# Optimization experiments

Hardware: AMD Instinct MI355X
Metric: run time of the kernel (lower is better)

Reference implementation:

```python
import jax, jax.numpy as jnp
import numpy as np

B, L, D, H, F = 4, 2048, 768, 12, 3072
ROUTE_FRAC = 0.15
LN_EPS = 1e-5


def _ln(x, g, b):
    m = jnp.mean(x, axis=-1, keepdims=True)
    v = jnp.mean((x - m) ** 2, axis=-1, keepdims=True)
    return (x - m) * jax.lax.rsqrt(v + LN_EPS) * g + b


def setup_inputs() -> dict:
    key = jax.random.key(0)
    ks = jax.random.split(key, 20)
    s = 0.02
    return {
        "hidden_states": jax.random.normal(ks[0], (B, L, D), dtype=jnp.float32),
        "g1": jnp.ones((D,), jnp.float32), "b1": jnp.zeros((D,), jnp.float32),
        "g2": jnp.ones((D,), jnp.float32), "b2": jnp.zeros((D,), jnp.float32),
        "Wr": jax.random.normal(ks[1], (D,), jnp.float32) * s, "br": jnp.zeros((), jnp.float32),
        "Wq": jax.random.normal(ks[2], (D, D), jnp.float32) * s, "bq": jnp.zeros((D,), jnp.float32),
        "Wk": jax.random.normal(ks[3], (D, D), jnp.float32) * s, "bk": jnp.zeros((D,), jnp.float32),
        "Wv": jax.random.normal(ks[4], (D, D), jnp.float32) * s, "bv": jnp.zeros((D,), jnp.float32),
        "Wo": jax.random.normal(ks[5], (D, D), jnp.float32) * s, "bo": jnp.zeros((D,), jnp.float32),
        "Wm": jax.random.normal(ks[6], (D, D), jnp.float32) * s, "bm": jnp.zeros((D,), jnp.float32),
        "W1": jax.random.normal(ks[7], (D, F), jnp.float32) * s, "bf1": jnp.zeros((F,), jnp.float32),
        "W2": jax.random.normal(ks[8], (F, D), jnp.float32) * s, "bf2": jnp.zeros((D,), jnp.float32),
    }


def reference(hidden_states, g1, b1, g2, b2, Wr, br, Wq, bq, Wk, bk, Wv, bv, Wo, bo, Wm, bm, W1, bf1, W2, bf2):
    b, l, d = hidden_states.shape
    dh = d // H
    normed = _ln(hidden_states, g1, b1)  # [B,L,D]

    # Router: per-token coherence score; lowest-coherence route_frac tokens get attention.
    scores = jax.nn.sigmoid(jnp.einsum('bld,d->bl', normed, Wr) + br)  # [B,L]
    k = max(1, int(round(ROUTE_FRAC * l)))
    _, idx = jax.lax.top_k(-scores, k)  # lowest-coherence token indices
    attn_mask = jnp.zeros((b, l), bool).at[jnp.arange(b)[:, None], idx].set(True)

    # Attention path (computed densely over all tokens, as the torch module does).
    q = (normed @ Wq + bq).reshape(b, l, H, dh)
    kk = (normed @ Wk + bk).reshape(b, l, H, dh)
    v = (normed @ Wv + bv).reshape(b, l, H, dh)
    logits = jnp.einsum('blhd,bmhd->bhlm', q, kk) / jnp.sqrt(jnp.float32(dh))
    probs = jax.nn.softmax(logits, axis=-1)
    ctx = jnp.einsum('bhlm,bmhd->blhd', probs, v).reshape(b, l, d)
    attn_out = ctx @ Wo + bo

    # Lightweight coherence-mixing path: coherence-weighted global pooling + linear.
    w = scores / (jnp.sum(scores, axis=1, keepdims=True) + 1e-6)
    pooled = jnp.einsum('bl,bld->bd', w, normed)  # [B,D]
    mix_out = (normed + scores[..., None] * pooled[:, None, :]) @ Wm + bm

    merged = jnp.where(attn_mask[..., None], attn_out, mix_out)
    h = hidden_states + merged  # dropout is identity at eval

    n2 = _ln(h, g2, b2)
    ffn = jax.nn.gelu(n2 @ W1 + bf1, approximate=False) @ W2 + bf2
    return h + ffn
```

## Files before the change

### kernel.cpp

```cpp
#include <hip/hip_runtime.h>
#include <math.h>

#define B_ 4
#define L_ 2048
#define D_ 768
#define H_ 12
#define F_ 3072
#define KTOP 307
#define KPAD 320
#define LN_EPS 1e-5f

typedef unsigned int u32;
typedef unsigned short u16;
using bf16x8 = __attribute__((ext_vector_type(8))) short;
using f32x4  = __attribute__((ext_vector_type(4))) float;

#define AS1 __attribute__((address_space(1)))
#define AS3 __attribute__((address_space(3)))

__device__ __forceinline__ void gl16(const void* g, void* l) {
    __builtin_amdgcn_global_load_lds((const AS1 u32*)g, (AS3 u32*)l, 16, 0, 0);
}
__device__ __forceinline__ void wait_vm0() {
    asm volatile("s_waitcnt vmcnt(0)" ::: "memory");
}
__device__ __forceinline__ u16 f2bf(float f) {
    u32 u = __float_as_uint(f);
    return (u16)((u + 0x7fff + ((u >> 16) & 1)) >> 16);
}
__device__ __forceinline__ float bf2f(u16 s) {
    return __uint_as_float(((u32)s) << 16);
}
__device__ __forceinline__ float gelu_tanh(float v) {
    float u = v * v * v;
    float z = fmaf(u, 0.0713548163f, 1.59576912f * v);
    float s = __builtin_amdgcn_rcpf(1.0f + __expf(-z));
    return v * s;
}

__device__ __forceinline__ float blk_reduce_sum(float v, float* red) {
    #pragma unroll
    for (int off = 32; off; off >>= 1) v += __shfl_xor(v, off, 64);
    __syncthreads();
    if ((threadIdx.x & 63) == 0) red[threadIdx.x >> 6] = v;
    __syncthreads();
    return red[0] + red[1] + red[2] + red[3];
}

template <bool SCORE>
__global__ __launch_bounds__(256) void ln_kernel(
    const float* __restrict__ x, const float* __restrict__ g,
    const float* __restrict__ be, const float* __restrict__ Wr,
    const float* __restrict__ brp, u16* __restrict__ outn,
    float* __restrict__ scores)
{
    __shared__ float red[4];
    const int t = blockIdx.x;
    const int tid = threadIdx.x;
    const float* xr = x + (size_t)t * D_;
    float v0 = xr[tid], v1 = xr[tid + 256], v2 = xr[tid + 512];
    float mean = blk_reduce_sum(v0 + v1 + v2, red) * (1.0f / 768.0f);
    float d0 = v0 - mean, d1 = v1 - mean, d2 = v2 - mean;
    __syncthreads();
    float var = blk_reduce_sum(d0 * d0 + d1 * d1 + d2 * d2, red) * (1.0f / 768.0f);
    float inv = 1.0f / sqrtf(var + LN_EPS);
    float n0 = d0 * inv * g[tid] + be[tid];
    float n1 = d1 * inv * g[tid + 256] + be[tid + 256];
    float n2 = d2 * inv * g[tid + 512] + be[tid + 512];
    u16* orow = outn + (size_t)t * D_;
    orow[tid] = f2bf(n0); orow[tid + 256] = f2bf(n1); orow[tid + 512] = f2bf(n2);
    if (SCORE) {
        __syncthreads();
        float dot = blk_reduce_sum(n0 * Wr[tid] + n1 * Wr[tid + 256] + n2 * Wr[tid + 512], red);
        if (tid == 0) scores[t] = 1.0f / (1.0f + expf(-(dot + brp[0])));
    }
}

__global__ __launch_bounds__(1024) void topk_kernel(
    const float* __restrict__ scores, unsigned* __restrict__ mask,
    float* __restrict__ ssum, int* __restrict__ rowmap, int* __restrict__ inv)
{
    __shared__ u32 sb[L_];
    __shared__ u32 hist[256];
    __shared__ u32 wsum[16];
    __shared__ float redf[16];
    __shared__ u32 bcast[2];
    __shared__ u32 cnt_sel;
    const int b = blockIdx.x, tid = threadIdx.x;
    const int lane = tid & 63, wv = tid >> 6;

    if (tid == 0) cnt_sel = 0;
    float s0 = scores[b * L_ + tid];
    float s1 = scores[b * L_ + tid + 1024];
    sb[tid] = __float_as_uint(s0);
    sb[tid + 1024] = __float_as_uint(s1);
    float v = s0 + s1;
    #pragma unroll
    for (int o = 32; o; o >>= 1) v += __shfl_xor(v, o, 64);
    if (lane == 0) redf[wv] = v;
    __syncthreads();
    if (tid == 0) {
        float t = 0.f;
        #pragma unroll
        for (int w = 0; w < 16; w++) t += redf[w];
        ssum[b] = t;
    }

    u32 want = KTOP, prefix = 0;
    #pragma unroll
    for (int pass = 0; pass < 4; pass++) {
        const int shift = 24 - pass * 8;
        if (tid < 256) hist[tid] = 0;
        __syncthreads();
        u32 x0 = sb[tid], x1 = sb[tid + 1024];
        if (pass == 0 || (x0 >> (shift + 8)) == prefix) atomicAdd(&hist[(x0 >> shift) & 255], 1u);
        if (pass == 0 || (x1 >> (shift + 8)) == prefix) atomicAdd(&hist[(x1 >> shift) & 255], 1u);
        __syncthreads();
        u32 c = 0, inc = 0;
        if (tid < 256) {
            c = hist[tid];
            inc = c;
            #pragma unroll
            for (int o = 1; o < 64; o <<= 1) {
                u32 t = __shfl_up(inc, o, 64);
                if (lane >= o) inc += t;
            }
            if (lane == 63) wsum[wv] = inc;
        }
        __syncthreads();
        if (tid < 256) {
            u32 base = 0;
            #pragma unroll
            for (int w = 0; w < 4; w++) if (w < wv) base += wsum[w];
            u32 incl = base + inc;
            u32 excl = incl - c;
            if (excl < want && want <= incl) {
                bcast[0] = (u32)tid;
                bcast[1] = want - excl;
            }
        }
        __syncthreads();
        prefix = (prefix << 8) | bcast[0];
        want = bcast[1];
    }

    const u32 sstar = prefix;
    u32 a0 = sb[2 * tid], a1 = sb[2 * tid + 1];
    u32 e0 = (a0 == sstar) ? 1u : 0u, e1 = (a1 == sstar) ? 1u : 0u;
    u32 ps = e0 + e1, inc2 = ps;
    #pragma unroll
    for (int o = 1; o < 64; o <<= 1) {
        u32 t = __shfl_up(inc2, o, 64);
        if (lane >= o) inc2 += t;
    }
    __syncthreads();
    if (lane == 63) wsum[wv] = inc2;
    __syncthreads();
    u32 base = 0;
    #pragma unroll
    for (int w = 0; w < 16; w++) if (w < wv) base += wsum[w];
    u32 excl0 = base + inc2 - ps;
    {
        int i = 2 * tid;
        bool sel = (a0 < sstar) || (e0 && (excl0 < want));
        mask[b * L_ + i] = sel ? 1u : 0u;
        int invv = 0;
        if (sel) {
            u32 slot = atomicAdd(&cnt_sel, 1u);
            rowmap[b * KPAD + slot] = b * L_ + i;
            invv = b * KPAD + (int)slot;
        }
        inv[b * L_ + i] = invv;
    }
    {
        int i = 2 * tid + 1;
        u32 r1 = excl0 + e0;
        bool sel = (a1 < sstar) || (e1 && (r1 < want));
        mask[b * L_ + i] = sel ? 1u : 0u;
        int invv = 0;
        if (sel) {
            u32 slot = atomicAdd(&cnt_sel, 1u);
            rowmap[b * KPAD + slot] = b * L_ + i;
            invv = b * KPAD + (int)slot;
        }
        inv[b * L_ + i] = invv;
    }
    if (tid < KPAD - KTOP)
        rowmap[b * KPAD + KTOP + tid] = b * L_;
}

__global__ __launch_bounds__(256) void pooled_part(
    const float* __restrict__ scores, const u16* __restrict__ nb,
    float* __restrict__ parts)
{
    const int lc = blockIdx.x, b = blockIdx.y, tid = threadIdx.x;
    float a0 = 0.f, a1 = 0.f, a2 = 0.f;
    for (int l = lc * 256; l < lc * 256 + 256; l++) {
        float s = scores[b * L_ + l];
        const u16* row = nb + (size_t)(b * L_ + l) * D_;
        a0 += s * bf2f(row[tid]);
        a1 += s * bf2f(row[tid + 256]);
        a2 += s * bf2f(row[tid + 512]);
    }
    float* p = parts + (size_t)(lc * B_ + b) * D_;
    p[tid] = a0; p[tid + 256] = a1; p[tid + 512] = a2;
}

__global__ __launch_bounds__(256) void pooled_wm(
    const float* __restrict__ parts, const float* __restrict__ ssum,
    const float* __restrict__ Wm, float* __restrict__ pWm)
{
    __shared__ float pl[768];
    const int b = blockIdx.y, n0 = blockIdx.x * 256, tid = threadIdx.x;
    float inv = 1.0f / (ssum[b] + 1e-6f);
    for (int d = tid; d < 768; d += 256) {
        float s = 0.f;
        #pragma unroll
        for (int lc = 0; lc < 8; lc++) s += parts[(size_t)(lc * B_ + b) * D_ + d];
        pl[d] = s * inv;
    }
    __syncthreads();
    const int n = n0 + tid;
    float acc = 0.f;
    for (int k = 0; k < 768; k++) acc += pl[k] * Wm[(size_t)k * D_ + n];
    pWm[b * D_ + n] = acc;
}

__global__ __launch_bounds__(256) void wconv_all(
    const float* __restrict__ Wq, const float* __restrict__ Wk,
    const float* __restrict__ Wv, const float* __restrict__ Wo,
    const float* __restrict__ Wm, const float* __restrict__ W1,
    const float* __restrict__ W2,
    u16* __restrict__ WqT, u16* __restrict__ WkvT, u16* __restrict__ WoT,
    u16* __restrict__ WmT, u16* __restrict__ W1T, u16* __restrict__ W2T,
    const float* __restrict__ bq, const float* __restrict__ bk,
    const float* __restrict__ bv, float* __restrict__ bqs,
    float* __restrict__ bkv)
{
    __shared__ float t[32][33];
    int id = blockIdx.x;
    const int tid = threadIdx.x;
    if (id >= 7488) {
        for (int i = tid; i < 768; i += 256) {
            bqs[i] = bq[i] * 0.125f;
            bkv[i] = bk[i];
            bkv[768 + i] = bv[i];
        }
        return;
    }
    const float* src; u16* dst; int K, N, local; float sc = 1.f;
    if (id < 576)       { src = Wq; dst = WqT; K = 768; N = 768; local = id; sc = 0.125f; }
    else if (id < 1152) { src = Wk; dst = WkvT;            K = 768; N = 768; local = id - 576; }
    else if (id < 1728) { src = Wv; dst = WkvT + 768 * 768; K = 768; N = 768; local = id - 1152; }
    else if (id < 2304) { src = Wo; dst = WoT; K = 768; N = 768; local = id - 1728; }
    else if (id < 2880) { src = Wm; dst = WmT; K = 768; N = 768; local = id - 2304; }
    else if (id < 5184) { src = W1; dst = W1T; K = 768; N = 3072; local = id - 2880; }
    else                { src = W2; dst = W2T; K = 3072; N = 768; local = id - 5184; }
    const int ntiles = N >> 5;
    const int n0 = (local % ntiles) * 32, k0 = (local / ntiles) * 32;
    const int tx = tid & 31, ty = tid >> 5;
    #pragma unroll
    for (int i = 0; i < 4; i++)
        t[ty + i * 8][tx] = src[(size_t)(k0 + ty + i * 8) * N + n0 + tx];
    __syncthreads();
    #pragma unroll
    for (int i = 0; i < 4; i++)
        dst[(size_t)(n0 + ty + i * 8) * K + k0 + tx] = f2bf(t[tx][ty + i * 8] * sc);
}

template <int EPI, bool RMAP, int TM>
__global__ __launch_bounds__(256) void mfma_gemm(
    const u16* __restrict__ A, const u16* __restrict__ Bt,
    const float* __restrict__ bias, void* __restrict__ Cout,
    int N, int K, int nbn,
    const float* __restrict__ x, const unsigned* __restrict__ msk,
    const float* __restrict__ attn, const float* __restrict__ scores,
    const float* __restrict__ pWm, const float* __restrict__ hres,
    const int* __restrict__ rowmap, const int* __restrict__ invmap)
{
    constexpr int NI = (TM == 128) ? 4 : 2;
    constexpr int ASLOTS = TM * 8 / 256;
    __shared__ u16 Asm[TM * 64];
    __shared__ u16 Bsm[128 * 64];
    const int tid = threadIdx.x;
    const int wave = tid >> 6, lane = tid & 63;
    const int quad = lane >> 4, l15 = lane & 15;

    const int wid = blockIdx.x;
    const int m0 = (wid / nbn) * TM, n0 = (wid % nbn) * 128;
    const int wm = (TM == 128) ? (wave >> 1) * 64 : 0;
    const int wn = (TM == 128) ? (wave & 1) * 64 : wave * 32;

    f32x4 acc[4][NI];
    #pragma unroll
    for (int i = 0; i < 4; i++)
        #pragma unroll
        for (int j = 0; j < NI; j++) acc[i][j] = 0.f;

    const u16* ap[ASLOTS]; const u16* bp[4];
    #pragma unroll
    for (int i = 0; i < ASLOTS; i++) {
        int s = i * 256 + tid;
        int row = s >> 3;
        int kq = (s & 7) ^ (row & 7);
        int arow = RMAP ? rowmap[m0 + row] : (m0 + row);
        ap[i] = A + (size_t)arow * K + kq * 8;
    }
    #pragma unroll
    for (int i = 0; i < 4; i++) {
        int s = i * 256 + tid;
        int row = s >> 3;
        int kq = (s & 7) ^ (row & 7);
        bp[i] = Bt + (size_t)(n0 + row) * K + kq * 8;
    }

    for (int k0 = 0; k0 < K; k0 += 64) {
        #pragma unroll
        for (int i = 0; i < ASLOTS; i++) {
            gl16(ap[i], &Asm[(i * 256 + wave * 64) * 8]);
            ap[i] += 64;
        }
        #pragma unroll
        for (int i = 0; i < 4; i++) {
            gl16(bp[i], &Bsm[(i * 256 + wave * 64) * 8]);
            bp[i] += 64;
        }
        wait_vm0();
        __syncthreads();
        #pragma unroll
        for (int kk = 0; kk < 2; kk++) {
            bf16x8 af[4], bf[NI];
            const int kq = kk * 4 + quad;
            #pragma unroll
            for (int mi = 0; mi < 4; mi++) {
                int row = wm + mi * 16 + l15;
                af[mi] = *(const bf16x8*)&Asm[(row * 8 + (kq ^ (row & 7))) * 8];
            }
            #pragma unroll
            for (int ni = 0; ni < NI; ni++) {
                int row = wn + ni * 16 + l15;
                bf[ni] = *(const bf16x8*)&Bsm[(row * 8 + (kq ^ (row & 7))) * 8];
            }
            #pragma unroll
            for (int mi = 0; mi < 4; mi++)
                #pragma unroll
                for (int ni = 0; ni < NI; ni++)
                    acc[mi][ni] = __builtin_amdgcn_mfma_f32_16x16x32_bf16(
                        af[mi], bf[ni], acc[mi][ni], 0, 0, 0);
        }
        __syncthreads();
    }

    #pragma unroll
    for (int mi = 0; mi < 4; mi++) {
        #pragma unroll
        for (int ni = 0; ni < NI; ni++) {
            #pragma unroll
            for (int r = 0; r < 4; r++) {
                int row = m0 + wm + mi * 16 + quad * 4 + r;
                int col = n0 + wn + ni * 16 + l15;
                float v = acc[mi][ni][r] + bias[col];
                size_t off = (size_t)row * N + col;
                if (EPI == 0) ((float*)Cout)[off] = v;
                else if (EPI == 1) ((u16*)Cout)[off] = f2bf(v);
                else if (EPI == 2) ((u16*)Cout)[off] = f2bf(gelu_tanh(v));
                else if (EPI == 3) {
                    float mix = v + scores[row] * pWm[(row >> 11) * D_ + col];
                    float sel = msk[row] ? attn[(size_t)invmap[row] * D_ + col] : mix;
                    ((float*)Cout)[off] = x[off] + sel;
                } else {
                    ((float*)Cout)[off] = v + hres[off];
                }
            }
        }
    }
}

__global__ __launch_bounds__(256) void vtrans(
    const u16* __restrict__ V, u16* __restrict__ VT, int ld)
{
    __shared__ u16 tl[64 * 72];
    const int tid = threadIdx.x;
    const int l0 = blockIdx.x * 64, h = blockIdx.y, b = blockIdx.z;
    const u16* src = V + h * 64;
    {
        int r = tid >> 3, ch = tid & 7;
        *(uint4*)&tl[r * 72 + ch * 8] =
            *(const uint4*)&src[(size_t)(b * L_ + l0 + r) * ld + ch * 8];
        int t2 = tid + 256; r = t2 >> 3; ch = t2 & 7;
        *(uint4*)&tl[r * 72 + ch * 8] =
            *(const uint4*)&src[(size_t)(b * L_ + l0 + r) * ld + ch * 8];
    }
    __syncthreads();
    int d = tid >> 2, lg = (tid & 3) * 16;
    u16* dst = VT + (size_t)((b * H_ + h) * 64 + d) * L_ + l0 + lg;
    union { u16 s[8]; uint4 v; } pk;
    #pragma unroll
    for (int j = 0; j < 8; j++) pk.s[j] = tl[(lg + j) * 72 + d];
    *(uint4*)dst = pk.v;
    #pragma unroll
    for (int j = 0; j < 8; j++) pk.s[j] = tl[(lg + 8 + j) * 72 + d];
    *(uint4*)(dst + 8) = pk.v;
}

__global__ __launch_bounds__(256) void attn2(
    const u16* __restrict__ qcomp, const u16* __restrict__ Kg,
    const u16* __restrict__ VTg, u16* __restrict__ ctxc)
{
    __shared__ u16 Qs[64 * 64];
    __shared__ u16 Ks[64 * 64];
    __shared__ u16 Vs[64 * 64];
    __shared__ u16 Ps[4 * 16 * 72];
    const int tid = threadIdx.x, wave = tid >> 6, lane = tid & 63;
    const int quad = lane >> 4, l15 = lane & 15;
    const int qb = blockIdx.x, h = blockIdx.y, b = blockIdx.z;
    const int q0 = qb * 64;

    {
        int s0 = wave * 64 + lane;
        int r = s0 >> 3, c = (s0 & 7) ^ (r & 7);
        gl16(qcomp + (size_t)(b * KPAD + q0 + r) * D_ + h * 64 + c * 8,
             &Qs[(wave * 64) * 8]);
        int s1 = s0 + 256;
        int r1 = s1 >> 3, c1 = (s1 & 7) ^ (r1 & 7);
        gl16(qcomp + (size_t)(b * KPAD + q0 + r1) * D_ + h * 64 + c1 * 8,
             &Qs[(256 + wave * 64) * 8]);
    }
    const u16 *kp0, *kp1, *vp0, *vp1;
    {
        int s0 = wave * 64 + lane;
        int r = s0 >> 3, c = (s0 & 7) ^ (r & 7);
        kp0 = Kg + (size_t)(b * L_ + r) * 1536 + h * 64 + c * 8;
        vp0 = VTg + (size_t)((b * H_ + h) * 64 + r) * L_ + c * 8;
        int s1 = s0 + 256;
        int r1 = s1 >> 3, c1 = (s1 & 7) ^ (r1 & 7);
        kp1 = Kg + (size_t)(b * L_ + r1) * 1536 + h * 64 + c1 * 8;
        vp1 = VTg + (size_t)((b * H_ + h) * 64 + r1) * L_ + c1 * 8;
    }
    wait_vm0();
    __syncthreads();
    bf16x8 qf0, qf1;
    {
        int row = wave * 16 + l15;
        qf0 = *(const bf16x8*)&Qs[(row * 8 + ((quad)     ^ (row & 7))) * 8];
        qf1 = *(const bf16x8*)&Qs[(row * 8 + ((4 + quad) ^ (row & 7))) * 8];
    }
    f32x4 accO[4]; float lp[4];
    #pragma unroll
    for (int i = 0; i < 4; i++) { accO[i] = 0.f; lp[i] = 0.f; }
    u16* Psw = Ps + wave * 16 * 72;

    for (int kt = 0; kt < L_; kt += 64) {
        gl16(kp0, &Ks[(wave * 64) * 8]);        kp0 += (size_t)64 * 1536;
        gl16(kp1, &Ks[(256 + wave * 64) * 8]);  kp1 += (size_t)64 * 1536;
        gl16(vp0, &Vs[(wave * 64) * 8]);        vp0 += 64;
        gl16(vp1, &Vs[(256 + wave * 64) * 8]);  vp1 += 64;
        wait_vm0();
        __syncthreads();

        f32x4 accS[4];
        #pragma unroll
        for (int ni = 0; ni < 4; ni++) accS[ni] = 0.f;
        #pragma unroll
        for (int kk = 0; kk < 2; kk++) {
            const int kq = kk * 4 + quad;
            #pragma unroll
            for (int ni = 0; ni < 4; ni++) {
                int row = ni * 16 + l15;
                bf16x8 kf = *(const bf16x8*)&Ks[(row * 8 + (kq ^ (row & 7))) * 8];
                accS[ni] = __builtin_amdgcn_mfma_f32_16x16x32_bf16(
                    kk ? qf1 : qf0, kf, accS[ni], 0, 0, 0);
            }
        }
        #pragma unroll
        for (int ni = 0; ni < 4; ni++) {
            #pragma unroll
            for (int r = 0; r < 4; r++) {
                float p = __expf(accS[ni][r]);
                lp[r] += p;
                Psw[(quad * 4 + r) * 72 + ni * 16 + l15] = f2bf(p);
            }
        }
        #pragma unroll
        for (int kk = 0; kk < 2; kk++) {
            bf16x8 pf = *(const bf16x8*)&Psw[l15 * 72 + kk * 32 + quad * 8];
            const int kq = kk * 4 + quad;
            #pragma unroll
            for (int ni = 0; ni < 4; ni++) {
                int row = ni * 16 + l15;
                bf16x8 vf = *(const bf16x8*)&Vs[(row * 8 + (kq ^ (row & 7))) * 8];
                accO[ni] = __builtin_amdgcn_mfma_f32_16x16x32_bf16(pf, vf, accO[ni], 0, 0, 0);
            }
        }
        __syncthreads();
    }

    float invl[4];
    #pragma unroll
    for (int r = 0; r < 4; r++) {
        float s = lp[r];
        s += __shfl_xor(s, 1, 64); s += __shfl_xor(s, 2, 64);
        s += __shfl_xor(s, 4, 64); s += __shfl_xor(s, 8, 64);
        invl[r] = 1.0f / s;
    }
    #pragma unroll
    for (int ni = 0; ni < 4; ni++) {
        #pragma unroll
        for (int r = 0; r < 4; r++) {
            int ql = q0 + wave * 16 + quad * 4 + r;
            if (ql < KTOP)
                ctxc[(size_t)(b * KPAD + ql) * D_ + h * 64 + ni * 16 + l15] =
                    f2bf(accO[ni][r] * invl[r]);
        }
    }
}

extern "C" void kernel_launch(void* const* d_in, const int* in_sizes, int n_in,
                              void* d_out, int out_size, void* d_ws, size_t ws_size,
                              hipStream_t stream)
{
    const float* x   = (const float*)d_in[0];
    const float* g1  = (const float*)d_in[1];
    const float* b1  = (const float*)d_in[2];
    const float* g2  = (const float*)d_in[3];
    const float* b2  = (const float*)d_in[4];
    const float* Wr  = (const float*)d_in[5];
    const float* br  = (const float*)d_in[6];
    const float* Wq  = (const float*)d_in[7];
    const float* bq  = (const float*)d_in[8];
    const float* Wk  = (const float*)d_in[9];
    const float* bk  = (const float*)d_in[10];
    const float* Wv  = (const float*)d_in[11];
    const float* bv  = (const float*)d_in[12];
    const float* Wo  = (const float*)d_in[13];
    const float* bo  = (const float*)d_in[14];
    const float* Wm  = (const float*)d_in[15];
    const float* bm  = (const float*)d_in[16];
    const float* W1  = (const float*)d_in[17];
    const float* bf1 = (const float*)d_in[18];
    const float* W2  = (const float*)d_in[19];
    const float* bf2 = (const float*)d_in[20];
    float* out = (float*)d_out;

    char* W = (char*)d_ws;
    u16* WqT  = (u16*)(W + 0);
    u16* WkvT = (u16*)(W + 1179648);
    u16* WoT  = (u16*)(W + 3538944);
    u16* WmT  = (u16*)(W + 4718592);
    u16* W1T  = (u16*)(W + 5898240);
    u16* W2T  = (u16*)(W + 10616832);
    float* scores  = (float*)(W + 15335424);
    unsigned* mask = (unsigned*)(W + 15368192);
    float* ssum    = (float*)(W + 15400960);
    float* pWm     = (float*)(W + 15413504);
    float* parts   = (float*)(W + 15425792);
    float* bkv     = (float*)(W + 15524096);
    float* bqs     = (float*)(W + 15530240);
    int* rowmap    = (int*)(W + 15533312);
    int* invmap    = (int*)(W + 15538432);
    u16* nb    = (u16*)(W + 15728640);
    u16* Y     = (u16*)(W + 28311552);
    u16* qcomp = (u16*)(W + 53477376);
    u16* ctxc  = (u16*)(W + 55443456);
    float* attnc = (float*)(W + 57409536);
    u16* VT    = (u16*)(W + 61341696);
    float* h   = (float*)(W + 28311552);
    u16* n2b   = (u16*)(W + 15728640);
    u16* mid   = (u16*)(W + 53477376);

    wconv_all<<<7489, 256, 0, stream>>>(Wq, Wk, Wv, Wo, Wm, W1, W2,
                                        WqT, WkvT, WoT, WmT, W1T, W2T,
                                        bq, bk, bv, bqs, bkv);

    const int NT = B_ * L_;
    ln_kernel<true><<<NT, 256, 0, stream>>>(x, g1, b1, Wr, br, nb, scores);
    topk_kernel<<<B_, 1024, 0, stream>>>(scores, mask, ssum, rowmap, invmap);
    pooled_part<<<dim3(8, B_), 256, 0, stream>>>(scores, nb, parts);
    pooled_wm<<<dim3(3, B_), 256, 0, stream>>>(parts, ssum, Wm, pWm);

    mfma_gemm<1, false, 128><<<768, 256, 0, stream>>>(nb, WkvT, bkv, Y, 1536, 768, 12,
        nullptr, nullptr, nullptr, nullptr, nullptr, nullptr, nullptr, nullptr);
    mfma_gemm<1, true, 64><<<120, 256, 0, stream>>>(nb, WqT, bqs, qcomp, 768, 768, 6,
        nullptr, nullptr, nullptr, nullptr, nullptr, nullptr, rowmap, nullptr);
    vtrans<<<dim3(32, H_, B_), 256, 0, stream>>>(Y + 768, VT, 1536);
    attn2<<<dim3(KPAD / 64, H_, B_), 256, 0, stream>>>(qcomp, Y, VT, ctxc);
    mfma_gemm<0, false, 64><<<120, 256, 0, stream>>>(ctxc, WoT, bo, attnc, 768, 768, 6,
        nullptr, nullptr, nullptr, nullptr, nullptr, nullptr, nullptr, nullptr);
    mfma_gemm<3, false, 64><<<768, 256, 0, stream>>>(nb, WmT, bm, h, 768, 768, 6,
        x, mask, attnc, scores, pWm, nullptr, nullptr, invmap);
    ln_kernel<false><<<NT, 256, 0, stream>>>(h, g2, b2, nullptr, nullptr, n2b, nullptr);
    mfma_gemm<2, false, 128><<<1536, 256, 0, stream>>>(n2b, W1T, bf1, mid, 3072, 768, 24,
        nullptr, nullptr, nullptr, nullptr, nullptr, nullptr, nullptr, nullptr);
    mfma_gemm<4, false, 64><<<768, 256, 0, stream>>>(mid, W2T, bf2, out, 768, 3072, 6,
        nullptr, nullptr, nullptr, nullptr, nullptr, h, nullptr, nullptr);
}
```

Baseline: 466.6 us.

## Double-buffer LDS tiles in MFMA GEMM to overlap loads with compute

```diff
diff --git a/kernel.cpp b/kernel.cpp
--- a/kernel.cpp
+++ b/kernel.cpp
@@ -280,8 +280,8 @@
 {
     constexpr int NI = (TM == 128) ? 4 : 2;
     constexpr int ASLOTS = TM * 8 / 256;
-    __shared__ u16 Asm[TM * 64];
-    __shared__ u16 Bsm[128 * 64];
+    __shared__ u16 Asm[2][TM * 64];
+    __shared__ u16 Bsm[2][128 * 64];
     const int tid = threadIdx.x;
     const int wave = tid >> 6, lane = tid & 63;
     const int quad = lane >> 4, l15 = lane & 15;
@@ -314,41 +314,57 @@
         bp[i] = Bt + (size_t)(n0 + row) * K + kq * 8;
     }
 
-    for (int k0 = 0; k0 < K; k0 += 64) {
+    auto stage = [&](int buf) {
         #pragma unroll
         for (int i = 0; i < ASLOTS; i++) {
-            gl16(ap[i], &Asm[(i * 256 + wave * 64) * 8]);
+            gl16(ap[i], &Asm[buf][(i * 256 + wave * 64) * 8]);
             ap[i] += 64;
         }
         #pragma unroll
         for (int i = 0; i < 4; i++) {
-            gl16(bp[i], &Bsm[(i * 256 + wave * 64) * 8]);
+            gl16(bp[i], &Bsm[buf][(i * 256 + wave * 64) * 8]);
             bp[i] += 64;
         }
-        wait_vm0();
-        __syncthreads();
+    };
+    auto compute = [&](int buf) {
         #pragma unroll
         for (int kk = 0; kk < 2; kk++) {
-            bf16x8 af[4], bf[NI];
+            bf16x8 af[4], bfr[NI];
             const int kq = kk * 4 + quad;
             #pragma unroll
             for (int mi = 0; mi < 4; mi++) {
                 int row = wm + mi * 16 + l15;
-                af[mi] = *(const bf16x8*)&Asm[(row * 8 + (kq ^ (row & 7))) * 8];
+                af[mi] = *(const bf16x8*)&Asm[buf][(row * 8 + (kq ^ (row & 7))) * 8];
             }
             #pragma unroll
             for (int ni = 0; ni < NI; ni++) {
                 int row = wn + ni * 16 + l15;
-                bf[ni] = *(const bf16x8*)&Bsm[(row * 8 + (kq ^ (row & 7))) * 8];
+                bfr[ni] = *(const bf16x8*)&Bsm[buf][(row * 8 + (kq ^ (row & 7))) * 8];
             }
             #pragma unroll
             for (int mi = 0; mi < 4; mi++)
                 #pragma unroll
                 for (int ni = 0; ni < NI; ni++)
                     acc[mi][ni] = __builtin_amdgcn_mfma_f32_16x16x32_bf16(
-                        af[mi], bf[ni], acc[mi][ni], 0, 0, 0);
-        }
-        __syncthreads();
+                        af[mi], bfr[ni], acc[mi][ni], 0, 0, 0);
+        }
+    };
+
+    const int nt = K >> 6;
+    stage(0);
+    wait_vm0();
+    __syncthreads();
+    for (int t = 0; t < nt; t += 2) {
+        stage(1);
+        compute(0);
+        wait_vm0();
+        __syncthreads();
+        if (t + 2 < nt) stage(0);
+        compute(1);
+        if (t + 2 < nt) {
+            wait_vm0();
+            __syncthreads();
+        }
     }
 
     #pragma unroll
```

Result: no change. 460.3 us (-1.3%).
